# Optimization experiments

Hardware: AMD Instinct MI355X
Metric: run time of the kernel (lower is better)

Reference implementation:

```python
import jax, jax.numpy as jnp
import numpy as np
from jax import lax

B, CR, CS = 2, 256, 512
HR = WR = 64
HS = WS = 32
D_INNER, D_STATE, DT_RANK, D_CONV = 512, 16, 16, 3
EPS = 1e-5


def setup_inputs() -> dict:
    key = jax.random.key(0)
    ks = jax.random.split(key, 16)
    s = 0.02
    return {
        "resnet_feat": jax.random.normal(ks[0], (B, CR, HR, WR), jnp.float32),
        "scp_feat": jax.random.normal(ks[1], (B, CS, HS, WS), jnp.float32),
        "scp_proj_w": jax.random.normal(ks[2], (CR, CS), jnp.float32) * s,
        "scp_bn_g": jnp.ones((CR,), jnp.float32),
        "scp_bn_b": jnp.zeros((CR,), jnp.float32),
        "scp_bn_m": jax.random.normal(ks[3], (CR,), jnp.float32) * 0.1,
        "scp_bn_v": jax.random.uniform(ks[4], (CR,), jnp.float32, minval=0.5, maxval=1.5),
        "res_bn_g": jnp.ones((CR,), jnp.float32),
        "res_bn_b": jnp.zeros((CR,), jnp.float32),
        "res_bn_m": jax.random.normal(ks[5], (CR,), jnp.float32) * 0.1,
        "res_bn_v": jax.random.uniform(ks[6], (CR,), jnp.float32, minval=0.5, maxval=1.5),
        "ln_g": jnp.ones((CR,), jnp.float32),
        "ln_b": jnp.zeros((CR,), jnp.float32),
        "in_proj_w": jax.random.normal(ks[7], (2 * D_INNER, CR), jnp.float32) * s,
        "conv_w": jax.random.normal(ks[8], (D_INNER, 1, D_CONV), jnp.float32) * s,
        "conv_b": jnp.zeros((D_INNER,), jnp.float32),
        "x_proj_w": jax.random.normal(ks[9], (DT_RANK + 2 * D_STATE, D_INNER), jnp.float32) * s,
        "dt_proj_w": jax.random.normal(ks[10], (D_INNER, DT_RANK), jnp.float32) * s,
        "dt_proj_b": jnp.full((D_INNER,), -4.6, jnp.float32),  # softplus -> dt ~ 0.01
        "A_log": jnp.log(jnp.broadcast_to(jnp.arange(1, D_STATE + 1, dtype=jnp.float32), (D_INNER, D_STATE))),
        "D": jnp.ones((D_INNER,), jnp.float32),
        "out_proj_w": jax.random.normal(ks[11], (CR, D_INNER), jnp.float32) * s,
    }


def _bn(x, g, b, m, v):
    # eval-mode BatchNorm2d with running stats, NCHW
    inv = g / jnp.sqrt(v + EPS)
    return x * inv[None, :, None, None] + (b - m * inv)[None, :, None, None]


def reference(resnet_feat, scp_feat, scp_proj_w, scp_bn_g, scp_bn_b, scp_bn_m, scp_bn_v,
              res_bn_g, res_bn_b, res_bn_m, res_bn_v, ln_g, ln_b, in_proj_w, conv_w, conv_b,
              x_proj_w, dt_proj_w, dt_proj_b, A_log, D, out_proj_w):
    # --- fusion prelude ---
    rn = _bn(resnet_feat, res_bn_g, res_bn_b, res_bn_m, res_bn_v)
    sp = jnp.einsum('bchw,oc->bohw', scp_feat, scp_proj_w)        # 1x1 conv, no bias
    sp = _bn(sp, scp_bn_g, scp_bn_b, scp_bn_m, scp_bn_v)
    sp = jax.image.resize(sp, (B, CR, HR, WR), method='bilinear')  # align_corners=False semantics
    fused = rn + sp                                               # (B, CR, HR, WR)

    # --- Mamba2DBlock ---
    L = HR * WR
    x_seq = fused.transpose(0, 2, 3, 1).reshape(B, L, CR)
    mu = x_seq.mean(-1, keepdims=True)
    var = x_seq.var(-1, keepdims=True)
    xn = (x_seq - mu) / jnp.sqrt(var + EPS) * ln_g + ln_b         # LayerNorm

    xz = xn @ in_proj_w.T                                         # (B, L, 2*d_inner)
    xm, z = jnp.split(xz, 2, axis=-1)

    # causal depthwise conv1d over sequence
    xc = xm.transpose(0, 2, 1)                                    # (B, d_inner, L)
    xc = jnp.pad(xc, ((0, 0), (0, 0), (D_CONV - 1, 0)))
    xc = lax.conv_general_dilated(xc, conv_w, (1,), 'VALID',
                                  dimension_numbers=('NCH', 'OIH', 'NCH'),
                                  feature_group_count=D_INNER) + conv_b[None, :, None]
    u = jax.nn.silu(xc.transpose(0, 2, 1))                        # (B, L, d_inner)

    x_dbl = u @ x_proj_w.T                                        # (B, L, dt_rank + 2*d_state)
    dt_in, Bc, Cc = jnp.split(x_dbl, [DT_RANK, DT_RANK + D_STATE], axis=-1)
    dt = jax.nn.softplus(dt_in @ dt_proj_w.T + dt_proj_b)         # (B, L, d_inner)

    A = -jnp.exp(A_log)                                           # (d_inner, d_state)
    dA = jnp.exp(dt[..., None] * A)                               # (B, L, d_inner, d_state)
    dBu = dt[..., None] * Bc[:, :, None, :] * u[..., None]        # (B, L, d_inner, d_state)

    def comb(c1, c2):
        a1, b1 = c1
        a2, b2 = c2
        return a1 * a2, a2 * b1 + b2

    _, h = lax.associative_scan(comb, (dA, dBu), axis=1)          # h: (B, L, d_inner, d_state)
    y = jnp.einsum('blds,bls->bld', h, Cc) + u * D
    y = y * jax.nn.silu(z)
    out_seq = y @ out_proj_w.T                                    # (B, L, CR)
    out = out_seq.reshape(B, HR, WR, CR).transpose(0, 3, 1, 2)
    return fused + out
```

## Files before the change

### kernel.cpp

```cpp
#include <hip/hip_runtime.h>
#include <hip/hip_bf16.h>
#include <math.h>

typedef unsigned short u16;
typedef __attribute__((ext_vector_type(8))) short short8;
typedef __attribute__((ext_vector_type(4))) float f32x4;
typedef __attribute__((ext_vector_type(4))) unsigned short u16x4;

#define DEVINL static __device__ __forceinline__

DEVINL float b2f(u16 x) {
    union { unsigned u; float f; } v; v.u = ((unsigned)x) << 16; return v.f;
}
DEVINL u16 f2b(float f) {
    union { unsigned u; float f; } v; v.f = f;
    unsigned u = v.u;
    return (u16)((u + 0x7fffu + ((u >> 16) & 1u)) >> 16);
}
DEVINL float silu(float x) { return x * __fdividef(1.f, 1.f + __expf(-x)); }
DEVINL float ld_any(bool f32, const void* p, size_t i) {
    return f32 ? ((const float*)p)[i] : b2f(((const u16*)p)[i]);
}
template<bool F32> DEVINL float LDs(const void* p, size_t i) {
    if constexpr (F32) return ((const float*)p)[i];
    else               return b2f(((const u16*)p)[i]);
}

DEVINL bool detect_f32(const u16* __restrict__ raw) {
    int cnt = 0;
#pragma unroll
    for (int i = 0; i < 64; ++i) {
        float v = b2f(raw[i * 2]);
        if (!(fabsf(v) <= 1e3f)) cnt++;
    }
    return cnt > 0;
}

#define O_INW  0
#define O_XPW  262144
#define O_OPW  286720
#define O_SPW  417792
#define O_CW   548864
#define O_CB   550400
#define O_DTW  550912
#define O_ALOG 559104
#define O_DTB  567296
#define O_DW   567808
#define O_SG   568320
#define O_SB   568576
#define O_SM   568832
#define O_SV   569088
#define O_RG   569344
#define O_RB   569600
#define O_RM   569856
#define O_RV   570112
#define O_LG   570368
#define O_LB   570624
#define N_CVT  570880
#define O_FLAG 570880

DEVINL void tr_tile(bool f32, const void* src, u16* dst, int R, int C,
                    int c0, int r0, int b, int tid)
{
    __shared__ u16 t[64][66];
    int lane = tid & 63, grp = tid >> 6;
#pragma unroll
    for (int j = 0; j < 16; ++j) {
        int rl = j * 4 + grp;
        t[rl][lane] = f2b(ld_any(f32, src, ((size_t)b * R + r0 + rl) * C + c0 + lane));
    }
    __syncthreads();
#pragma unroll
    for (int j = 0; j < 16; ++j) {
        int cl = j * 4 + grp;
        dst[((size_t)b * C + c0 + cl) * R + r0 + lane] = t[lane][cl];
    }
}

__global__ __launch_bounds__(256) void k_prep(
    const void* inw, const void* xpw, const void* opw, const void* spw,
    const void* cw, const void* cb, const void* dtw, const void* alog,
    const void* dtb, const void* Dw,
    const void* sg, const void* sb, const void* sm, const void* sv,
    const void* rg, const void* rb, const void* rm, const void* rv,
    const void* lg, const void* lb,
    const void* scp, const void* resnet,
    u16* __restrict__ w16, u16* __restrict__ scpT, u16* __restrict__ resnetT)
{
    bool f32 = detect_f32((const u16*)resnet);
    int bid = blockIdx.x, tid = threadIdx.x;
    if (bid < 2230) {
        int i = bid * 256 + tid;
        const void* src; int off = i;
        if      (i < O_XPW)  { src = inw; }
        else if (i < O_OPW)  { src = xpw;  off = i - O_XPW; }
        else if (i < O_SPW)  { src = opw;  off = i - O_OPW; }
        else if (i < O_CW)   { src = spw;  off = i - O_SPW; }
        else if (i < O_CB)   { src = cw;   off = i - O_CW; }
        else if (i < O_DTW)  { src = cb;   off = i - O_CB; }
        else if (i < O_ALOG) { src = dtw;  off = i - O_DTW; }
        else if (i < O_DTB)  { src = alog; off = i - O_ALOG; }
        else if (i < O_DW)   { src = dtb;  off = i - O_DTB; }
        else if (i < O_SG)   { src = Dw;   off = i - O_DW; }
        else if (i < O_SB)   { src = sg;   off = i - O_SG; }
        else if (i < O_SM)   { src = sb;   off = i - O_SB; }
        else if (i < O_SV)   { src = sm;   off = i - O_SM; }
        else if (i < O_RG)   { src = sv;   off = i - O_SV; }
        else if (i < O_RB)   { src = rg;   off = i - O_RG; }
        else if (i < O_RM)   { src = rb;   off = i - O_RB; }
        else if (i < O_RV)   { src = rm;   off = i - O_RM; }
        else if (i < O_LG)   { src = rv;   off = i - O_RV; }
        else if (i < O_LB)   { src = lg;   off = i - O_LG; }
        else                 { src = lb;   off = i - O_LB; }
        w16[i] = f2b(ld_any(f32, src, off));
    } else if (bid < 2230 + 256) {
        int t = bid - 2230;
        tr_tile(f32, scp, scpT, 512, 1024, (t & 15) * 64, ((t >> 4) & 7) * 64, t >> 7, tid);
    } else if (bid < 2998) {
        int t = bid - 2486;
        tr_tile(f32, resnet, resnetT, 256, 4096, (t & 63) * 64, ((t >> 6) & 3) * 64, t >> 8, tid);
    } else {
        __shared__ int oksh;
        if (tid == 0) oksh = 1;
        __syncthreads();
        bool ok = true;
        for (int i = tid; i < 512 * 16; i += 256) {
            int s = i & 15;
            float av = -__expf(ld_any(f32, alog, i));
            if (fabsf(av + (float)(s + 1)) > 0.03f * (float)(s + 1)) ok = false;
        }
        if (!ok) atomicAnd(&oksh, 0);
        __syncthreads();
        if (tid == 0) w16[O_FLAG] = (u16)oksh;
    }
}

__global__ __launch_bounds__(256) void k_scpmm(
    const u16* __restrict__ scpT, const u16* __restrict__ w16,
    u16* __restrict__ sp16)
{
    const int N = 256, K = 512;
    int tid = threadIdx.x, lane = tid & 63, wid = tid >> 6;
    int ln = lane & 15, q = lane >> 4;
    int m0 = blockIdx.x * 64 + (wid & 1) * 32;
    int n0 = blockIdx.y * 64 + (wid >> 1) * 32;
    f32x4 acc00 = {0.f,0.f,0.f,0.f}, acc01 = acc00, acc10 = acc00, acc11 = acc00;
    const u16* Ap0 = scpT + (size_t)(m0 + ln) * K + q * 8;
    const u16* Ap1 = Ap0 + (size_t)16 * K;
    const u16* Wp = w16 + O_SPW;
#pragma unroll 4
    for (int k0 = 0; k0 < K; k0 += 32) {
        int kk = k0 + q * 8;
        short8 a0 = *reinterpret_cast<const short8*>(Ap0 + k0);
        short8 a1 = *reinterpret_cast<const short8*>(Ap1 + k0);
        short8 b0 = *reinterpret_cast<const short8*>(Wp + (size_t)(n0 + ln) * K + kk);
        short8 b1 = *reinterpret_cast<const short8*>(Wp + (size_t)(n0 + ln + 16) * K + kk);
        acc00 = __builtin_amdgcn_mfma_f32_16x16x32_bf16(a0, b0, acc00, 0, 0, 0);
        acc01 = __builtin_amdgcn_mfma_f32_16x16x32_bf16(a0, b1, acc01, 0, 0, 0);
        acc10 = __builtin_amdgcn_mfma_f32_16x16x32_bf16(a1, b0, acc10, 0, 0, 0);
        acc11 = __builtin_amdgcn_mfma_f32_16x16x32_bf16(a1, b1, acc11, 0, 0, 0);
    }
    int r0 = m0 + q * 4, c0 = n0 + ln;
    float inv0 = b2f(w16[O_SG + c0]) * rsqrtf(b2f(w16[O_SV + c0]) + 1e-5f);
    float sh0  = b2f(w16[O_SB + c0]) - b2f(w16[O_SM + c0]) * inv0;
    float inv1 = b2f(w16[O_SG + c0 + 16]) * rsqrtf(b2f(w16[O_SV + c0 + 16]) + 1e-5f);
    float sh1  = b2f(w16[O_SB + c0 + 16]) - b2f(w16[O_SM + c0 + 16]) * inv1;
#pragma unroll
    for (int r = 0; r < 4; ++r) {
        sp16[(size_t)(r0 + r) * N + c0]           = f2b(acc00[r] * inv0 + sh0);
        sp16[(size_t)(r0 + r) * N + c0 + 16]      = f2b(acc01[r] * inv1 + sh1);
        sp16[(size_t)(r0 + 16 + r) * N + c0]      = f2b(acc10[r] * inv0 + sh0);
        sp16[(size_t)(r0 + 16 + r) * N + c0 + 16] = f2b(acc11[r] * inv1 + sh1);
    }
}

__global__ __launch_bounds__(256) void k_ln(
    const u16* __restrict__ resnetT, const u16* __restrict__ w16,
    const u16* __restrict__ sp16, u16* __restrict__ xn)
{
    __shared__ float red[8];
    int c = threadIdx.x, b = blockIdx.y;
    float inv = b2f(w16[O_RG + c]) * rsqrtf(b2f(w16[O_RV + c]) + 1e-5f);
    float sh  = b2f(w16[O_RB + c]) - b2f(w16[O_RM + c]) * inv;
    float lgv = b2f(w16[O_LG + c]), lbv = b2f(w16[O_LB + c]);
    const u16* spc = sp16 + (size_t)b * 1024 * 256 + c;
    for (int j = 0; j < 8; ++j) {
        int l = blockIdx.x * 8 + j;
        int h = l >> 6, w = l & 63;
        float rr = b2f(resnetT[((size_t)b * 4096 + l) * 256 + c]);
        float rn = rr * inv + sh;
        float xh = 0.5f * h - 0.25f; int jh = (int)floorf(xh); float fh = xh - jh;
        float xw = 0.5f * w - 0.25f; int jw = (int)floorf(xw); float fw = xw - jw;
        int h0 = jh < 0 ? 0 : jh, h1 = jh + 1 > 31 ? 31 : jh + 1;
        int w0 = jw < 0 ? 0 : jw, w1 = jw + 1 > 31 ? 31 : jw + 1;
        float v00 = b2f(spc[(size_t)(h0 * 32 + w0) * 256]), v01 = b2f(spc[(size_t)(h0 * 32 + w1) * 256]);
        float v10 = b2f(spc[(size_t)(h1 * 32 + w0) * 256]), v11 = b2f(spc[(size_t)(h1 * 32 + w1) * 256]);
        float sp = (1.f - fh) * ((1.f - fw) * v00 + fw * v01)
                 + fh * ((1.f - fw) * v10 + fw * v11);
        float fv = rn + sp;

        float s = fv, s2 = fv * fv;
#pragma unroll
        for (int off = 1; off < 64; off <<= 1) {
            s  += __shfl_xor(s, off);
            s2 += __shfl_xor(s2, off);
        }
        int wv = c >> 6;
        if ((c & 63) == 0) { red[wv] = s; red[4 + wv] = s2; }
        __syncthreads();
        float S  = red[0] + red[1] + red[2] + red[3];
        float S2 = red[4] + red[5] + red[6] + red[7];
        __syncthreads();
        float mu   = S * (1.f / 256.f);
        float var  = S2 * (1.f / 256.f) - mu * mu;
        float rstd = rsqrtf(var + 1e-5f);
        xn[((size_t)b * 4096 + l) * 256 + c] = f2b((fv - mu) * rstd * lgv + lbv);
    }
}

__global__ __launch_bounds__(256) void k_gemm_in(
    const u16* __restrict__ A, const u16* __restrict__ w16, u16* __restrict__ Out)
{
    const int N = 1024, K = 256;
    int tid = threadIdx.x, lane = tid & 63, wid = tid >> 6;
    int ln = lane & 15, q = lane >> 4;
    int m0 = blockIdx.x * 128 + (wid & 1) * 64;
    int n0 = blockIdx.y * 128 + (wid >> 1) * 64;
    f32x4 acc[4][4];
#pragma unroll
    for (int i = 0; i < 4; ++i)
#pragma unroll
        for (int j = 0; j < 4; ++j) acc[i][j] = {0.f,0.f,0.f,0.f};
    const u16* Ap = A + (size_t)(m0 + ln) * K + q * 8;
    const u16* Bp = w16 + O_INW + (size_t)(n0 + ln) * K + q * 8;
#pragma unroll
    for (int k0 = 0; k0 < K; k0 += 32) {
        short8 a[4], bb[4];
#pragma unroll
        for (int i = 0; i < 4; ++i)
            a[i] = *reinterpret_cast<const short8*>(Ap + (size_t)(16 * i) * K + k0);
#pragma unroll
        for (int j = 0; j < 4; ++j)
            bb[j] = *reinterpret_cast<const short8*>(Bp + (size_t)(16 * j) * K + k0);
#pragma unroll
        for (int i = 0; i < 4; ++i)
#pragma unroll
            for (int j = 0; j < 4; ++j)
                acc[i][j] = __builtin_amdgcn_mfma_f32_16x16x32_bf16(a[i], bb[j], acc[i][j], 0, 0, 0);
    }
    int r0 = m0 + q * 4, c0 = n0 + ln;
#pragma unroll
    for (int i = 0; i < 4; ++i)
#pragma unroll
        for (int j = 0; j < 4; ++j)
#pragma unroll
            for (int r = 0; r < 4; ++r)
                Out[(size_t)(r0 + 16 * i + r) * N + c0 + 16 * j] = f2b(acc[i][j][r]);
}

DEVINL short8 u_frag(const u16* __restrict__ xz, const u16* __restrict__ w16,
                     int row, int kk0)
{
    int l = row & 4095;
    const u16* p = xz + (size_t)row * 1024 + kk0;
    short8 zz = {0,0,0,0,0,0,0,0};
    short8 x0 = *reinterpret_cast<const short8*>(p);
    short8 x1 = (l >= 1) ? *reinterpret_cast<const short8*>(p - 1024) : zz;
    short8 x2 = (l >= 2) ? *reinterpret_cast<const short8*>(p - 2048) : zz;
    short8 r;
#pragma unroll
    for (int j = 0; j < 8; ++j) {
        int d = kk0 + j;
        float acc = b2f(w16[O_CB + d])
                  + b2f((u16)x2[j]) * b2f(w16[O_CW + d * 3])
                  + b2f((u16)x1[j]) * b2f(w16[O_CW + d * 3 + 1])
                  + b2f((u16)x0[j]) * b2f(w16[O_CW + d * 3 + 2]);
        r[j] = (short)f2b(silu(acc));
    }
    return r;
}

__global__ __launch_bounds__(128) void k_xproj(
    const u16* __restrict__ xz, const u16* __restrict__ w16, float* __restrict__ xdf)
{
    int tid = threadIdx.x, lane = tid & 63, wid = tid >> 6;
    int ln = lane & 15, q = lane >> 4;
    int m0 = blockIdx.x * 32 + wid * 16;
    const u16* Wp = w16 + O_XPW;
    f32x4 acc[3];
#pragma unroll
    for (int j = 0; j < 3; ++j) acc[j] = {0.f,0.f,0.f,0.f};
    for (int k0 = 0; k0 < 512; k0 += 32) {
        int kk0 = k0 + q * 8;
        short8 a0 = u_frag(xz, w16, m0 + ln, kk0);
#pragma unroll
        for (int j = 0; j < 3; ++j) {
            short8 bj = *reinterpret_cast<const short8*>(Wp + (size_t)(16 * j + ln) * 512 + kk0);
            acc[j] = __builtin_amdgcn_mfma_f32_16x16x32_bf16(a0, bj, acc[j], 0, 0, 0);
        }
    }
#pragma unroll
    for (int j = 0; j < 3; ++j)
#pragma unroll
        for (int r = 0; r < 4; ++r)
            xdf[(size_t)(m0 + q * 4 + r) * 48 + 16 * j + ln] = acc[j][r];
}


#define SCAN_PRELUDE()                                                        \
    const float* xr = xr0 + (size_t)il * 48;                                  \
    float x0 = b2f(xz[xbase + (size_t)il * 1024]);                            \
    float uv = silu(cbv + cw0 * x2 + cw1 * x1 + cw2 * x0);                    \
    float pa = 0.f, pb = 0.f, pc = 0.f, pq = 0.f;                             \
    _Pragma("unroll")                                                         \
    for (int j = 0; j < 4; ++j) {                                             \
        pa += xr[j]      * wdt[j];      pb += xr[4 + j]  * wdt[4 + j];        \
        pc += xr[8 + j]  * wdt[8 + j];  pq += xr[12 + j] * wdt[12 + j];       \
    }                                                                         \
    float accd = bias + ((pa + pb) + (pc + pq));                              \
    float dtv = accd > 15.f ? accd : __logf(1.f + __expf(accd));              \
    float du = dtv * uv;

__global__ __launch_bounds__(512) void k_scan1(
    const u16* __restrict__ xz, const float* __restrict__ xdf,
    const u16* __restrict__ w16, unsigned* __restrict__ cAH,
    int NC, int CL)
{
    int d = threadIdx.x, ck = blockIdx.x, b = blockIdx.y;
    float wdt[16];
#pragma unroll
    for (int j = 0; j < 16; ++j) wdt[j] = b2f(w16[O_DTW + d * 16 + j]);
    float bias = b2f(w16[O_DTB + d]);
    float cw0 = b2f(w16[O_CW + d * 3]), cw1 = b2f(w16[O_CW + d * 3 + 1]),
          cw2 = b2f(w16[O_CW + d * 3 + 2]), cbv = b2f(w16[O_CB + d]);
    int l0 = ck * CL;
    size_t xbase = ((size_t)b * 4096 + l0) * 1024 + d;
    float x2 = (l0 >= 2) ? b2f(xz[xbase - 2048]) : 0.f;
    float x1 = (l0 >= 1) ? b2f(xz[xbase - 1024]) : 0.f;
    const float* xr0 = xdf + ((size_t)b * 4096 + l0) * 48;
    size_t obase = (((size_t)b * NC + ck) * 16) * 512 + d;
    float h[16];
#pragma unroll
    for (int s = 0; s < 16; ++s) h[s] = 0.f;

    if (w16[O_FLAG]) {
        float sdt = 0.f;
#pragma unroll 2
        for (int il = 0; il < CL; ++il) {
            SCAN_PRELUDE();
            sdt += dtv;
            float e1 = __expf(-dtv);
            float e2 = e1 * e1, e3 = e2 * e1, e4 = e2 * e2;
            float e8 = e4 * e4, e12 = e8 * e4;
            float inn[4] = {e1, e2, e3, e4};
            float bas[4] = {1.f, e4, e8, e12};
#pragma unroll
            for (int s = 0; s < 16; ++s)
                h[s] = (bas[s >> 2] * inn[s & 3]) * h[s] + du * xr[16 + s];
            x2 = x1; x1 = x0;
        }
        float E1 = __expf(-sdt);
        float E2 = E1 * E1, E3 = E2 * E1, E4 = E2 * E2;
        float E8 = E4 * E4, E12 = E8 * E4;
        float iN[4] = {E1, E2, E3, E4};
        float bA[4] = {1.f, E4, E8, E12};
#pragma unroll
        for (int s = 0; s < 16; ++s)
            cAH[obase + (size_t)s * 512] =
                (unsigned)f2b(bA[s >> 2] * iN[s & 3]) | ((unsigned)f2b(h[s]) << 16);
    } else {
        float a[16], ap[16];
#pragma unroll
        for (int s = 0; s < 16; ++s) {
            a[s] = -__expf(b2f(w16[O_ALOG + d * 16 + s]));
            ap[s] = 1.f;
        }
        for (int il = 0; il < CL; ++il) {
            SCAN_PRELUDE();
#pragma unroll
            for (int s = 0; s < 16; ++s) {
                float dA = __expf(dtv * a[s]);
                h[s] = dA * h[s] + du * xr[16 + s];
                ap[s] *= dA;
            }
            x2 = x1; x1 = x0;
        }
#pragma unroll
        for (int s = 0; s < 16; ++s)
            cAH[obase + (size_t)s * 512] =
                (unsigned)f2b(ap[s]) | ((unsigned)f2b(h[s]) << 16);
    }
}

__global__ __launch_bounds__(128) void k_scan2(
    const unsigned* __restrict__ cAH, u16* __restrict__ hIn, int NC)
{
    int d = blockIdx.y * 128 + threadIdx.x, s = blockIdx.x, b = blockIdx.z;
    float h = 0.f;
#pragma unroll 8
    for (int ck = 0; ck < NC; ++ck) {
        size_t idx = (((size_t)b * NC + ck) * 16 + s) * 512 + d;
        unsigned v = cAH[idx];
        float aP = b2f((u16)(v & 0xffffu));
        float hE = b2f((u16)(v >> 16));
        hIn[idx] = f2b(h);
        h = aP * h + hE;
    }
}

__global__ __launch_bounds__(512) void k_scan3(
    const u16* __restrict__ xz, const float* __restrict__ xdf,
    const u16* __restrict__ w16, const u16* __restrict__ hIn,
    u16* __restrict__ y, int NC, int CL)
{
    int d = threadIdx.x, ck = blockIdx.x, b = blockIdx.y;
    float wdt[16];
#pragma unroll
    for (int j = 0; j < 16; ++j) wdt[j] = b2f(w16[O_DTW + d * 16 + j]);
    float bias = b2f(w16[O_DTB + d]);
    float Dv = b2f(w16[O_DW + d]);
    float cw0 = b2f(w16[O_CW + d * 3]), cw1 = b2f(w16[O_CW + d * 3 + 1]),
          cw2 = b2f(w16[O_CW + d * 3 + 2]), cbv = b2f(w16[O_CB + d]);
    int l0 = ck * CL;
    size_t xbase = ((size_t)b * 4096 + l0) * 1024 + d;
    float x2 = (l0 >= 2) ? b2f(xz[xbase - 2048]) : 0.f;
    float x1 = (l0 >= 1) ? b2f(xz[xbase - 1024]) : 0.f;
    const float* xr0 = xdf + ((size_t)b * 4096 + l0) * 48;
    size_t obase = (((size_t)b * NC + ck) * 16) * 512 + d;
    float h[16];
#pragma unroll
    for (int s = 0; s < 16; ++s) h[s] = b2f(hIn[obase + (size_t)s * 512]);

    if (w16[O_FLAG]) {
#pragma unroll 2
        for (int il = 0; il < CL; ++il) {
            SCAN_PRELUDE();
            float e1 = __expf(-dtv);
            float e2 = e1 * e1, e3 = e2 * e1, e4 = e2 * e2;
            float e8 = e4 * e4, e12 = e8 * e4;
            float inn[4] = {e1, e2, e3, e4};
            float bas[4] = {1.f, e4, e8, e12};
            float yv = 0.f;
#pragma unroll
            for (int s = 0; s < 16; ++s) {
                h[s] = (bas[s >> 2] * inn[s & 3]) * h[s] + du * xr[16 + s];
                yv += h[s] * xr[32 + s];
            }
            size_t row = (size_t)b * 4096 + l0 + il;
            yv += uv * Dv;
            float zv = b2f(xz[row * 1024 + 512 + d]);
            yv *= silu(zv);
            y[row * 512 + d] = f2b(yv);
            x2 = x1; x1 = x0;
        }
    } else {
        float a[16];
#pragma unroll
        for (int s = 0; s < 16; ++s)
            a[s] = -__expf(b2f(w16[O_ALOG + d * 16 + s]));
        for (int il = 0; il < CL; ++il) {
            SCAN_PRELUDE();
            float yv = 0.f;
#pragma unroll
            for (int s = 0; s < 16; ++s) {
                float dA = __expf(dtv * a[s]);
                h[s] = dA * h[s] + du * xr[16 + s];
                yv += h[s] * xr[32 + s];
            }
            size_t row = (size_t)b * 4096 + l0 + il;
            yv += uv * Dv;
            float zv = b2f(xz[row * 1024 + 512 + d]);
            yv *= silu(zv);
            y[row * 512 + d] = f2b(yv);
            x2 = x1; x1 = x0;
        }
    }
}

template<bool F32> DEVINL void out_body(
    const u16* Y, const u16* w16, const void* resnet,
    const u16* sp16, void* outp)
{
    const int K = 512;
    int tid = threadIdx.x, lane = tid & 63, wid = tid >> 6;
    int ln = lane & 15, q = lane >> 4;
    int m0 = blockIdx.x * 64 + (wid & 1) * 32;
    int n0 = blockIdx.y * 128 + (wid >> 1) * 64;
    f32x4 acc[2][4];
#pragma unroll
    for (int i = 0; i < 2; ++i)
#pragma unroll
        for (int j = 0; j < 4; ++j) acc[i][j] = {0.f,0.f,0.f,0.f};
    const u16* Ap0 = w16 + O_OPW + (size_t)(m0 + ln) * K + q * 8;
    const u16* Ap1 = Ap0 + (size_t)16 * K;
    const u16* Bp  = Y + (size_t)(n0 + ln) * K + q * 8;
#pragma unroll 2
    for (int k0 = 0; k0 < K; k0 += 32) {
        short8 a0 = *reinterpret_cast<const short8*>(Ap0 + k0);
        short8 a1 = *reinterpret_cast<const short8*>(Ap1 + k0);
#pragma unroll
        for (int j = 0; j < 4; ++j) {
            short8 bj = *reinterpret_cast<const short8*>(Bp + (size_t)(16 * j) * K + k0);
            acc[0][j] = __builtin_amdgcn_mfma_f32_16x16x32_bf16(a0, bj, acc[0][j], 0, 0, 0);
            acc[1][j] = __builtin_amdgcn_mfma_f32_16x16x32_bf16(a1, bj, acc[1][j], 0, 0, 0);
        }
    }
    int r0 = m0 + q * 4;
    int nb = n0 + ln;
    float inv8[2][4], sh8[2][4];
#pragma unroll
    for (int im = 0; im < 2; ++im)
#pragma unroll
        for (int r = 0; r < 4; ++r) {
            int c = r0 + 16 * im + r;
            float inv = b2f(w16[O_RG + c]) * rsqrtf(b2f(w16[O_RV + c]) + 1e-5f);
            inv8[im][r] = inv;
            sh8[im][r]  = b2f(w16[O_RB + c]) - b2f(w16[O_RM + c]) * inv;
        }
#pragma unroll
    for (int jn = 0; jn < 4; ++jn) {
        int n = nb + 16 * jn;
        int b = n >> 12, l = n & 4095;
        int hh = l >> 6, w = l & 63;
        float xh = 0.5f * hh - 0.25f; int jh = (int)floorf(xh); float fh = xh - jh;
        float xw = 0.5f * w - 0.25f;  int jw = (int)floorf(xw); float fw = xw - jw;
        int h0 = jh < 0 ? 0 : jh, h1 = jh + 1 > 31 ? 31 : jh + 1;
        int w0 = jw < 0 ? 0 : jw, w1 = jw + 1 > 31 ? 31 : jw + 1;
        float w00 = (1.f - fh) * (1.f - fw), w01 = (1.f - fh) * fw;
        float w10 = fh * (1.f - fw),         w11 = fh * fw;
        const u16* spb = sp16 + (size_t)b * 1024 * 256;
#pragma unroll
        for (int im = 0; im < 2; ++im) {
            int cb = r0 + 16 * im;
            u16x4 s00 = *reinterpret_cast<const u16x4*>(spb + (size_t)(h0 * 32 + w0) * 256 + cb);
            u16x4 s01 = *reinterpret_cast<const u16x4*>(spb + (size_t)(h0 * 32 + w1) * 256 + cb);
            u16x4 s10 = *reinterpret_cast<const u16x4*>(spb + (size_t)(h1 * 32 + w0) * 256 + cb);
            u16x4 s11 = *reinterpret_cast<const u16x4*>(spb + (size_t)(h1 * 32 + w1) * 256 + cb);
#pragma unroll
            for (int r = 0; r < 4; ++r) {
                int c = cb + r;
                float rr = LDs<F32>(resnet, ((size_t)b * 256 + c) * 4096 + l);
                float sp = w00 * b2f(s00[r]) + w01 * b2f(s01[r])
                         + w10 * b2f(s10[r]) + w11 * b2f(s11[r]);
                float val = acc[im][jn][r] + rr * inv8[im][r] + sh8[im][r] + sp;
                size_t oi = ((size_t)b * 256 + c) * 4096 + l;
                if constexpr (F32) ((float*)outp)[oi] = val;
                else               ((u16*)outp)[oi]  = f2b(val);
            }
        }
    }
}
__global__ __launch_bounds__(256) void k_out(
    const u16* Y, const u16* w16, const void* resnet,
    const u16* sp16, void* outp)
{
    if (detect_f32((const u16*)resnet)) out_body<true>(Y, w16, resnet, sp16, outp);
    else                                out_body<false>(Y, w16, resnet, sp16, outp);
}

extern "C" void kernel_launch(void* const* d_in, const int* in_sizes, int n_in,
                              void* d_out, int out_size, void* d_ws, size_t ws_size,
                              hipStream_t stream)
{
    const void* resnet = d_in[0];
    const void* scp    = d_in[1];
    const void* spw    = d_in[2];
    const void* sg     = d_in[3];
    const void* sb     = d_in[4];
    const void* sm     = d_in[5];
    const void* sv     = d_in[6];
    const void* rg     = d_in[7];
    const void* rb     = d_in[8];
    const void* rm     = d_in[9];
    const void* rv     = d_in[10];
    const void* lg     = d_in[11];
    const void* lb     = d_in[12];
    const void* inw    = d_in[13];
    const void* cw     = d_in[14];
    const void* cb     = d_in[15];
    const void* xpw    = d_in[16];
    const void* dtw    = d_in[17];
    const void* dtb    = d_in[18];
    const void* alog   = d_in[19];
    const void* Dw     = d_in[20];
    const void* opw    = d_in[21];

    char*  ws      = (char*)d_ws;
    u16*   w16     = (u16*)(ws + 4096);
    u16*   sp16    = (u16*)(ws + 2097152);
    u16*   scpT    = (u16*)(ws + 4194304);
    u16*   resnetT = (u16*)(ws + 8388608);
    u16*   xn      = (u16*)(ws + 12582912);
    u16*   xz      = (u16*)(ws + 16777216);
    float* xdf     = (float*)(ws + 33554432);
    u16*   y       = (u16*)(ws + 35651584);
    const size_t tail0 = 44040192;

    int NC = 16;
    for (int cand = 256; cand >= 16; cand >>= 1) {
        if (tail0 + (size_t)cand * 98304 <= ws_size) { NC = cand; break; }
    }
    int CL = 4096 / NC;
    unsigned* cAH = (unsigned*)(ws + tail0);
    u16*      hIn = (u16*)(ws + tail0 + (size_t)NC * 65536);

    k_prep<<<dim3(2999), 256, 0, stream>>>(
        inw, xpw, opw, spw, cw, cb, dtw, alog, dtb, Dw,
        sg, sb, sm, sv, rg, rb, rm, rv, lg, lb,
        scp, resnet, w16, scpT, resnetT);
    k_scpmm<<<dim3(32, 4), 256, 0, stream>>>(scpT, w16, sp16);
    k_ln<<<dim3(512, 2), 256, 0, stream>>>(resnetT, w16, sp16, xn);
    k_gemm_in<<<dim3(64, 8), 256, 0, stream>>>(xn, w16, xz);
    k_xproj<<<dim3(256), 128, 0, stream>>>(xz, w16, xdf);
    k_scan1<<<dim3(NC, 2), 512, 0, stream>>>(xz, xdf, w16, cAH, NC, CL);
    k_scan2<<<dim3(16, 4, 2), 128, 0, stream>>>(cAH, hIn, NC);
    k_scan3<<<dim3(NC, 2), 512, 0, stream>>>(xz, xdf, w16, hIn, y, NC, CL);
    k_out<<<dim3(4, 64), 256, 0, stream>>>(y, w16, resnet, sp16, d_out);
}
```

Before: 250.3 us.

## Fuse all pipeline stages into one cooperative persistent kernel with grid syncs

Replaces nine separate kernel launches with a single cooperative kernel of 512 blocks of 512 threads. Every phase (prep, scp GEMM, LayerNorm, in-proj GEMM, x-proj, three scan passes, output) is remapped onto that fixed grid, with grid.sync between phases. Tile shapes are reworked to fit: gemm_in and out use narrower N tiles, and x-proj splits K across 4 waves with a shared-memory reduction. The scan chunk count is fixed at 256 instead of being chosen from workspace size. The aim is to remove launch gaps and tail effects, at the cost of grid-wide barriers, idle blocks in small phases, and 512-thread/occupancy register limits; there is a non-cooperative multi-launch fallback.

```diff
diff --git a/kernel.cpp b/kernel.cpp
--- a/kernel.cpp
+++ b/kernel.cpp
@@ -1,4 +1,5 @@
 #include <hip/hip_runtime.h>
+#include <hip/hip_cooperative_groups.h>
 #include <hip/hip_bf16.h>
 #include <math.h>
 
@@ -59,93 +60,102 @@
 #define N_CVT  570880
 #define O_FLAG 570880
 
-DEVINL void tr_tile(bool f32, const void* src, u16* dst, int R, int C,
-                    int c0, int r0, int b, int tid)
-{
-    __shared__ u16 t[64][66];
+#define NCK 256
+#define CLL 16
+
+struct KP {
+    const void *resnet, *scp, *spw, *sg, *sb, *sm, *sv, *rg, *rb, *rm, *rv,
+               *lg, *lb, *inw, *cw, *cb, *xpw, *dtw, *dtb, *alog, *Dw, *opw;
+    u16 *w16, *scpT, *resnetT, *xn, *sp16, *xz, *y, *hIn;
+    float *xdf;
+    unsigned *cAH;
+    void *outp;
+};
+
+DEVINL void tr_tile8(bool f32, const void* src, u16* dst, int R, int C,
+                     int c0, int r0, int b, int tid, u16 (*t)[66])
+{
     int lane = tid & 63, grp = tid >> 6;
 #pragma unroll
-    for (int j = 0; j < 16; ++j) {
-        int rl = j * 4 + grp;
+    for (int j = 0; j < 8; ++j) {
+        int rl = j * 8 + grp;
         t[rl][lane] = f2b(ld_any(f32, src, ((size_t)b * R + r0 + rl) * C + c0 + lane));
     }
     __syncthreads();
 #pragma unroll
-    for (int j = 0; j < 16; ++j) {
-        int cl = j * 4 + grp;
+    for (int j = 0; j < 8; ++j) {
+        int cl = j * 8 + grp;
         dst[((size_t)b * C + c0 + cl) * R + r0 + lane] = t[lane][cl];
     }
 }
 
-__global__ __launch_bounds__(256) void k_prep(
-    const void* inw, const void* xpw, const void* opw, const void* spw,
-    const void* cw, const void* cb, const void* dtw, const void* alog,
-    const void* dtb, const void* Dw,
-    const void* sg, const void* sb, const void* sm, const void* sv,
-    const void* rg, const void* rb, const void* rm, const void* rv,
-    const void* lg, const void* lb,
-    const void* scp, const void* resnet,
-    u16* __restrict__ w16, u16* __restrict__ scpT, u16* __restrict__ resnetT)
-{
-    bool f32 = detect_f32((const u16*)resnet);
-    int bid = blockIdx.x, tid = threadIdx.x;
-    if (bid < 2230) {
-        int i = bid * 256 + tid;
-        const void* src; int off = i;
-        if      (i < O_XPW)  { src = inw; }
-        else if (i < O_OPW)  { src = xpw;  off = i - O_XPW; }
-        else if (i < O_SPW)  { src = opw;  off = i - O_OPW; }
-        else if (i < O_CW)   { src = spw;  off = i - O_SPW; }
-        else if (i < O_CB)   { src = cw;   off = i - O_CW; }
-        else if (i < O_DTW)  { src = cb;   off = i - O_CB; }
-        else if (i < O_ALOG) { src = dtw;  off = i - O_DTW; }
-        else if (i < O_DTB)  { src = alog; off = i - O_ALOG; }
-        else if (i < O_DW)   { src = dtb;  off = i - O_DTB; }
-        else if (i < O_SG)   { src = Dw;   off = i - O_DW; }
-        else if (i < O_SB)   { src = sg;   off = i - O_SG; }
-        else if (i < O_SM)   { src = sb;   off = i - O_SB; }
-        else if (i < O_SV)   { src = sm;   off = i - O_SM; }
-        else if (i < O_RG)   { src = sv;   off = i - O_SV; }
-        else if (i < O_RB)   { src = rg;   off = i - O_RG; }
-        else if (i < O_RM)   { src = rb;   off = i - O_RB; }
-        else if (i < O_RV)   { src = rm;   off = i - O_RM; }
-        else if (i < O_LG)   { src = rv;   off = i - O_RV; }
-        else if (i < O_LB)   { src = lg;   off = i - O_LG; }
-        else                 { src = lb;   off = i - O_LB; }
-        w16[i] = f2b(ld_any(f32, src, off));
-    } else if (bid < 2230 + 256) {
-        int t = bid - 2230;
-        tr_tile(f32, scp, scpT, 512, 1024, (t & 15) * 64, ((t >> 4) & 7) * 64, t >> 7, tid);
-    } else if (bid < 2998) {
-        int t = bid - 2486;
-        tr_tile(f32, resnet, resnetT, 256, 4096, (t & 63) * 64, ((t >> 6) & 3) * 64, t >> 8, tid);
-    } else {
-        __shared__ int oksh;
-        if (tid == 0) oksh = 1;
+DEVINL void ph_prep(const KP& P, int blk, int tid, bool f32,
+                    u16 (*t)[66], int* sh_ok)
+{
+    u16* __restrict__ w16 = P.w16;
+    for (int id = blk; id < 1884; id += 512) {
+        if (id < 1115) {
+            int i = id * 512 + tid;
+            const void* src; int off = i;
+            if      (i < O_XPW)  { src = P.inw; }
+            else if (i < O_OPW)  { src = P.xpw;  off = i - O_XPW; }
+            else if (i < O_SPW)  { src = P.opw;  off = i - O_OPW; }
+            else if (i < O_CW)   { src = P.spw;  off = i - O_SPW; }
+            else if (i < O_CB)   { src = P.cw;   off = i - O_CW; }
+            else if (i < O_DTW)  { src = P.cb;   off = i - O_CB; }
+            else if (i < O_ALOG) { src = P.dtw;  off = i - O_DTW; }
+            else if (i < O_DTB)  { src = P.alog; off = i - O_ALOG; }
+            else if (i < O_DW)   { src = P.dtb;  off = i - O_DTB; }
+            else if (i < O_SG)   { src = P.Dw;   off = i - O_DW; }
+            else if (i < O_SB)   { src = P.sg;   off = i - O_SG; }
+            else if (i < O_SM)   { src = P.sb;   off = i - O_SB; }
+            else if (i < O_SV)   { src = P.sm;   off = i - O_SM; }
+            else if (i < O_RG)   { src = P.sv;   off = i - O_SV; }
+            else if (i < O_RB)   { src = P.rg;   off = i - O_RG; }
+            else if (i < O_RM)   { src = P.rb;   off = i - O_RB; }
+            else if (i < O_RV)   { src = P.rm;   off = i - O_RM; }
+            else if (i < O_LG)   { src = P.rv;   off = i - O_RV; }
+            else if (i < O_LB)   { src = P.lg;   off = i - O_LG; }
+            else                 { src = P.lb;   off = i - O_LB; }
+            w16[i] = f2b(ld_any(f32, src, off));
+        } else if (id < 1371) {
+            int tt = id - 1115;
+            tr_tile8(f32, P.scp, P.scpT, 512, 1024,
+                     (tt & 15) * 64, ((tt >> 4) & 7) * 64, tt >> 7, tid, t);
+        } else if (id < 1883) {
+            int tt = id - 1371;
+            tr_tile8(f32, P.resnet, P.resnetT, 256, 4096,
+                     (tt & 63) * 64, ((tt >> 6) & 3) * 64, tt >> 8, tid, t);
+        } else {
+            if (tid == 0) *sh_ok = 1;
+            __syncthreads();
+            bool ok = true;
+            for (int i = tid; i < 512 * 16; i += 512) {
+                int s = i & 15;
+                float av = -__expf(ld_any(f32, P.alog, i));
+                if (fabsf(av + (float)(s + 1)) > 0.03f * (float)(s + 1)) ok = false;
+            }
+            if (!ok) atomicAnd(sh_ok, 0);
+            __syncthreads();
+            if (tid == 0) w16[O_FLAG] = (u16)(*sh_ok);
+        }
         __syncthreads();
-        bool ok = true;
-        for (int i = tid; i < 512 * 16; i += 256) {
-            int s = i & 15;
-            float av = -__expf(ld_any(f32, alog, i));
-            if (fabsf(av + (float)(s + 1)) > 0.03f * (float)(s + 1)) ok = false;
-        }
-        if (!ok) atomicAnd(&oksh, 0);
-        __syncthreads();
-        if (tid == 0) w16[O_FLAG] = (u16)oksh;
-    }
-}
-
-__global__ __launch_bounds__(256) void k_scpmm(
-    const u16* __restrict__ scpT, const u16* __restrict__ w16,
-    u16* __restrict__ sp16)
-{
+    }
+}
+
+DEVINL void ph_scpmm(const KP& P, int blk, int tid)
+{
+    if (blk >= 128) return;
+    int lane = tid & 63, wid = tid >> 6;
+    if (wid >= 4) return;
+    const u16* __restrict__ w16 = P.w16;
     const int N = 256, K = 512;
-    int tid = threadIdx.x, lane = tid & 63, wid = tid >> 6;
     int ln = lane & 15, q = lane >> 4;
-    int m0 = blockIdx.x * 64 + (wid & 1) * 32;
-    int n0 = blockIdx.y * 64 + (wid >> 1) * 32;
+    int bx = blk & 31, by = blk >> 5;
+    int m0 = bx * 64 + (wid & 1) * 32;
+    int n0 = by * 64 + (wid >> 1) * 32;
     f32x4 acc00 = {0.f,0.f,0.f,0.f}, acc01 = acc00, acc10 = acc00, acc11 = acc00;
-    const u16* Ap0 = scpT + (size_t)(m0 + ln) * K + q * 8;
+    const u16* Ap0 = P.scpT + (size_t)(m0 + ln) * K + q * 8;
     const u16* Ap1 = Ap0 + (size_t)16 * K;
     const u16* Wp = w16 + O_SPW;
 #pragma unroll 4
@@ -167,27 +177,25 @@
     float sh1  = b2f(w16[O_SB + c0 + 16]) - b2f(w16[O_SM + c0 + 16]) * inv1;
 #pragma unroll
     for (int r = 0; r < 4; ++r) {
-        sp16[(size_t)(r0 + r) * N + c0]           = f2b(acc00[r] * inv0 + sh0);
-        sp16[(size_t)(r0 + r) * N + c0 + 16]      = f2b(acc01[r] * inv1 + sh1);
-        sp16[(size_t)(r0 + 16 + r) * N + c0]      = f2b(acc10[r] * inv0 + sh0);
-        sp16[(size_t)(r0 + 16 + r) * N + c0 + 16] = f2b(acc11[r] * inv1 + sh1);
-    }
-}
-
-__global__ __launch_bounds__(256) void k_ln(
-    const u16* __restrict__ resnetT, const u16* __restrict__ w16,
-    const u16* __restrict__ sp16, u16* __restrict__ xn)
-{
-    __shared__ float red[8];
-    int c = threadIdx.x, b = blockIdx.y;
+        P.sp16[(size_t)(r0 + r) * N + c0]           = f2b(acc00[r] * inv0 + sh0);
+        P.sp16[(size_t)(r0 + r) * N + c0 + 16]      = f2b(acc01[r] * inv1 + sh1);
+        P.sp16[(size_t)(r0 + 16 + r) * N + c0]      = f2b(acc10[r] * inv0 + sh0);
+        P.sp16[(size_t)(r0 + 16 + r) * N + c0 + 16] = f2b(acc11[r] * inv1 + sh1);
+    }
+}
+
+DEVINL void ph_ln(const KP& P, int blk, int tid, float (*red)[8])
+{
+    const u16* __restrict__ w16 = P.w16;
+    int sub = tid >> 8, c = tid & 255, b = sub;
     float inv = b2f(w16[O_RG + c]) * rsqrtf(b2f(w16[O_RV + c]) + 1e-5f);
     float sh  = b2f(w16[O_RB + c]) - b2f(w16[O_RM + c]) * inv;
     float lgv = b2f(w16[O_LG + c]), lbv = b2f(w16[O_LB + c]);
-    const u16* spc = sp16 + (size_t)b * 1024 * 256 + c;
+    const u16* spc = P.sp16 + (size_t)b * 1024 * 256 + c;
     for (int j = 0; j < 8; ++j) {
-        int l = blockIdx.x * 8 + j;
+        int l = blk * 8 + j;
         int h = l >> 6, w = l & 63;
-        float rr = b2f(resnetT[((size_t)b * 4096 + l) * 256 + c]);
+        float rr = b2f(P.resnetT[((size_t)b * 4096 + l) * 256 + c]);
         float rn = rr * inv + sh;
         float xh = 0.5f * h - 0.25f; int jh = (int)floorf(xh); float fh = xh - jh;
         float xw = 0.5f * w - 0.25f; int jw = (int)floorf(xw); float fw = xw - jw;
@@ -206,56 +214,56 @@
             s2 += __shfl_xor(s2, off);
         }
         int wv = c >> 6;
-        if ((c & 63) == 0) { red[wv] = s; red[4 + wv] = s2; }
+        if ((c & 63) == 0) { red[sub][wv] = s; red[sub][4 + wv] = s2; }
         __syncthreads();
-        float S  = red[0] + red[1] + red[2] + red[3];
-        float S2 = red[4] + red[5] + red[6] + red[7];
+        float S  = red[sub][0] + red[sub][1] + red[sub][2] + red[sub][3];
+        float S2 = red[sub][4] + red[sub][5] + red[sub][6] + red[sub][7];
         __syncthreads();
         float mu   = S * (1.f / 256.f);
         float var  = S2 * (1.f / 256.f) - mu * mu;
         float rstd = rsqrtf(var + 1e-5f);
-        xn[((size_t)b * 4096 + l) * 256 + c] = f2b((fv - mu) * rstd * lgv + lbv);
-    }
-}
-
-__global__ __launch_bounds__(256) void k_gemm_in(
-    const u16* __restrict__ A, const u16* __restrict__ w16, u16* __restrict__ Out)
-{
-    const int N = 1024, K = 256;
-    int tid = threadIdx.x, lane = tid & 63, wid = tid >> 6;
+        P.xn[((size_t)b * 4096 + l) * 256 + c] = f2b((fv - mu) * rstd * lgv + lbv);
+    }
+}
+
+DEVINL void ph_gemm_in(const KP& P, int blk, int tid)
+{
+    const int Nn = 1024, K = 256;
+    int lane = tid & 63, wid = tid >> 6;
     int ln = lane & 15, q = lane >> 4;
-    int m0 = blockIdx.x * 128 + (wid & 1) * 64;
-    int n0 = blockIdx.y * 128 + (wid >> 1) * 64;
-    f32x4 acc[4][4];
+    int bx = blk & 63, by = blk >> 6;
+    int m0 = bx * 128 + (wid & 1) * 64;
+    int n0 = by * 128 + (wid >> 1) * 32;
+    f32x4 acc[4][2];
 #pragma unroll
     for (int i = 0; i < 4; ++i)
 #pragma unroll
-        for (int j = 0; j < 4; ++j) acc[i][j] = {0.f,0.f,0.f,0.f};
-    const u16* Ap = A + (size_t)(m0 + ln) * K + q * 8;
-    const u16* Bp = w16 + O_INW + (size_t)(n0 + ln) * K + q * 8;
+        for (int j = 0; j < 2; ++j) acc[i][j] = {0.f,0.f,0.f,0.f};
+    const u16* Ap = P.xn + (size_t)(m0 + ln) * K + q * 8;
+    const u16* Bp = P.w16 + O_INW + (size_t)(n0 + ln) * K + q * 8;
 #pragma unroll
     for (int k0 = 0; k0 < K; k0 += 32) {
-        short8 a[4], bb[4];
+        short8 a[4], bb[2];
 #pragma unroll
         for (int i = 0; i < 4; ++i)
             a[i] = *reinterpret_cast<const short8*>(Ap + (size_t)(16 * i) * K + k0);
 #pragma unroll
-        for (int j = 0; j < 4; ++j)
+        for (int j = 0; j < 2; ++j)
             bb[j] = *reinterpret_cast<const short8*>(Bp + (size_t)(16 * j) * K + k0);
 #pragma unroll
         for (int i = 0; i < 4; ++i)
 #pragma unroll
-            for (int j = 0; j < 4; ++j)
+            for (int j = 0; j < 2; ++j)
                 acc[i][j] = __builtin_amdgcn_mfma_f32_16x16x32_bf16(a[i], bb[j], acc[i][j], 0, 0, 0);
     }
     int r0 = m0 + q * 4, c0 = n0 + ln;
 #pragma unroll
     for (int i = 0; i < 4; ++i)
 #pragma unroll
-        for (int j = 0; j < 4; ++j)
+        for (int j = 0; j < 2; ++j)
 #pragma unroll
             for (int r = 0; r < 4; ++r)
-                Out[(size_t)(r0 + 16 * i + r) * N + c0 + 16 * j] = f2b(acc[i][j][r]);
+                P.xz[(size_t)(r0 + 16 * i + r) * Nn + c0 + 16 * j] = f2b(acc[i][j][r]);
 }
 
 DEVINL short8 u_frag(const u16* __restrict__ xz, const u16* __restrict__ w16,
@@ -280,19 +288,21 @@
     return r;
 }
 
-__global__ __launch_bounds__(128) void k_xproj(
-    const u16* __restrict__ xz, const u16* __restrict__ w16, float* __restrict__ xdf)
-{
-    int tid = threadIdx.x, lane = tid & 63, wid = tid >> 6;
+DEVINL void ph_xproj(const KP& P, int blk, int tid, float (*xred)[4][64][12])
+{
+    if (blk >= 256) return;
+    int lane = tid & 63, wid = tid >> 6;
     int ln = lane & 15, q = lane >> 4;
-    int m0 = blockIdx.x * 32 + wid * 16;
-    const u16* Wp = w16 + O_XPW;
+    int grp = wid >> 2, wsub = wid & 3;
+    int m0 = blk * 32 + grp * 16;
+    const u16* Wp = P.w16 + O_XPW;
     f32x4 acc[3];
 #pragma unroll
     for (int j = 0; j < 3; ++j) acc[j] = {0.f,0.f,0.f,0.f};
-    for (int k0 = 0; k0 < 512; k0 += 32) {
+    int kb = wsub * 128;
+    for (int k0 = kb; k0 < kb + 128; k0 += 32) {
         int kk0 = k0 + q * 8;
-        short8 a0 = u_frag(xz, w16, m0 + ln, kk0);
+        short8 a0 = u_frag(P.xz, P.w16, m0 + ln, kk0);
 #pragma unroll
         for (int j = 0; j < 3; ++j) {
             short8 bj = *reinterpret_cast<const short8*>(Wp + (size_t)(16 * j + ln) * 512 + kk0);
@@ -302,10 +312,19 @@
 #pragma unroll
     for (int j = 0; j < 3; ++j)
 #pragma unroll
-        for (int r = 0; r < 4; ++r)
-            xdf[(size_t)(m0 + q * 4 + r) * 48 + 16 * j + ln] = acc[j][r];
-}
-
+        for (int r = 0; r < 4; ++r) xred[grp][wsub][lane][j * 4 + r] = acc[j][r];
+    __syncthreads();
+    if (wsub == 0) {
+#pragma unroll
+        for (int j = 0; j < 3; ++j)
+#pragma unroll
+            for (int r = 0; r < 4; ++r) {
+                float v = xred[grp][0][lane][j * 4 + r] + xred[grp][1][lane][j * 4 + r]
+                        + xred[grp][2][lane][j * 4 + r] + xred[grp][3][lane][j * 4 + r];
+                P.xdf[(size_t)(m0 + q * 4 + r) * 48 + 16 * j + ln] = v;
+            }
+    }
+}
 
 #define SCAN_PRELUDE()                                                        \
     const float* xr = xr0 + (size_t)il * 48;                                  \
@@ -321,24 +340,23 @@
     float dtv = accd > 15.f ? accd : __logf(1.f + __expf(accd));              \
     float du = dtv * uv;
 
-__global__ __launch_bounds__(512) void k_scan1(
-    const u16* __restrict__ xz, const float* __restrict__ xdf,
-    const u16* __restrict__ w16, unsigned* __restrict__ cAH,
-    int NC, int CL)
-{
-    int d = threadIdx.x, ck = blockIdx.x, b = blockIdx.y;
+DEVINL void ph_scan1(const KP& P, int blk, int tid)
+{
+    const u16* __restrict__ w16 = P.w16;
+    const u16* __restrict__ xz = P.xz;
+    int d = tid, ck = blk & 255, b = blk >> 8;
     float wdt[16];
 #pragma unroll
     for (int j = 0; j < 16; ++j) wdt[j] = b2f(w16[O_DTW + d * 16 + j]);
     float bias = b2f(w16[O_DTB + d]);
     float cw0 = b2f(w16[O_CW + d * 3]), cw1 = b2f(w16[O_CW + d * 3 + 1]),
           cw2 = b2f(w16[O_CW + d * 3 + 2]), cbv = b2f(w16[O_CB + d]);
-    int l0 = ck * CL;
+    int l0 = ck * CLL;
     size_t xbase = ((size_t)b * 4096 + l0) * 1024 + d;
     float x2 = (l0 >= 2) ? b2f(xz[xbase - 2048]) : 0.f;
     float x1 = (l0 >= 1) ? b2f(xz[xbase - 1024]) : 0.f;
-    const float* xr0 = xdf + ((size_t)b * 4096 + l0) * 48;
-    size_t obase = (((size_t)b * NC + ck) * 16) * 512 + d;
+    const float* xr0 = P.xdf + ((size_t)b * 4096 + l0) * 48;
+    size_t obase = (((size_t)b * NCK + ck) * 16) * 512 + d;
     float h[16];
 #pragma unroll
     for (int s = 0; s < 16; ++s) h[s] = 0.f;
@@ -346,7 +364,7 @@
     if (w16[O_FLAG]) {
         float sdt = 0.f;
 #pragma unroll 2
-        for (int il = 0; il < CL; ++il) {
+        for (int il = 0; il < CLL; ++il) {
             SCAN_PRELUDE();
             sdt += dtv;
             float e1 = __expf(-dtv);
@@ -366,7 +384,7 @@
         float bA[4] = {1.f, E4, E8, E12};
 #pragma unroll
         for (int s = 0; s < 16; ++s)
-            cAH[obase + (size_t)s * 512] =
+            P.cAH[obase + (size_t)s * 512] =
                 (unsigned)f2b(bA[s >> 2] * iN[s & 3]) | ((unsigned)f2b(h[s]) << 16);
     } else {
         float a[16], ap[16];
@@ -375,7 +393,7 @@
             a[s] = -__expf(b2f(w16[O_ALOG + d * 16 + s]));
             ap[s] = 1.f;
         }
-        for (int il = 0; il < CL; ++il) {
+        for (int il = 0; il < CLL; ++il) {
             SCAN_PRELUDE();
 #pragma unroll
             for (int s = 0; s < 16; ++s) {
@@ -387,33 +405,32 @@
         }
 #pragma unroll
         for (int s = 0; s < 16; ++s)
-            cAH[obase + (size_t)s * 512] =
+            P.cAH[obase + (size_t)s * 512] =
                 (unsigned)f2b(ap[s]) | ((unsigned)f2b(h[s]) << 16);
     }
 }
 
-__global__ __launch_bounds__(128) void k_scan2(
-    const unsigned* __restrict__ cAH, u16* __restrict__ hIn, int NC)
-{
-    int d = blockIdx.y * 128 + threadIdx.x, s = blockIdx.x, b = blockIdx.z;
+DEVINL void ph_scan2(const KP& P, int blk, int tid)
+{
+    if (blk >= 32) return;
+    int b = blk >> 4, s = blk & 15, d = tid;
     float h = 0.f;
 #pragma unroll 8
-    for (int ck = 0; ck < NC; ++ck) {
-        size_t idx = (((size_t)b * NC + ck) * 16 + s) * 512 + d;
-        unsigned v = cAH[idx];
+    for (int ck = 0; ck < NCK; ++ck) {
+        size_t idx = (((size_t)b * NCK + ck) * 16 + s) * 512 + d;
+        unsigned v = P.cAH[idx];
         float aP = b2f((u16)(v & 0xffffu));
         float hE = b2f((u16)(v >> 16));
-        hIn[idx] = f2b(h);
+        P.hIn[idx] = f2b(h);
         h = aP * h + hE;
     }
 }
 
-__global__ __launch_bounds__(512) void k_scan3(
-    const u16* __restrict__ xz, const float* __restrict__ xdf,
-    const u16* __restrict__ w16, const u16* __restrict__ hIn,
-    u16* __restrict__ y, int NC, int CL)
-{
-    int d = threadIdx.x, ck = blockIdx.x, b = blockIdx.y;
+DEVINL void ph_scan3(const KP& P, int blk, int tid)
+{
+    const u16* __restrict__ w16 = P.w16;
+    const u16* __restrict__ xz = P.xz;
+    int d = tid, ck = blk & 255, b = blk >> 8;
     float wdt[16];
 #pragma unroll
     for (int j = 0; j < 16; ++j) wdt[j] = b2f(w16[O_DTW + d * 16 + j]);
@@ -421,19 +438,19 @@
     float Dv = b2f(w16[O_DW + d]);
     float cw0 = b2f(w16[O_CW + d * 3]), cw1 = b2f(w16[O_CW + d * 3 + 1]),
           cw2 = b2f(w16[O_CW + d * 3 + 2]), cbv = b2f(w16[O_CB + d]);
-    int l0 = ck * CL;
+    int l0 = ck * CLL;
     size_t xbase = ((size_t)b * 4096 + l0) * 1024 + d;
     float x2 = (l0 >= 2) ? b2f(xz[xbase - 2048]) : 0.f;
     float x1 = (l0 >= 1) ? b2f(xz[xbase - 1024]) : 0.f;
-    const float* xr0 = xdf + ((size_t)b * 4096 + l0) * 48;
-    size_t obase = (((size_t)b * NC + ck) * 16) * 512 + d;
+    const float* xr0 = P.xdf + ((size_t)b * 4096 + l0) * 48;
+    size_t obase = (((size_t)b * NCK + ck) * 16) * 512 + d;
     float h[16];
 #pragma unroll
-    for (int s = 0; s < 16; ++s) h[s] = b2f(hIn[obase + (size_t)s * 512]);
+    for (int s = 0; s < 16; ++s) h[s] = b2f(P.hIn[obase + (size_t)s * 512]);
 
     if (w16[O_FLAG]) {
 #pragma unroll 2
-        for (int il = 0; il < CL; ++il) {
+        for (int il = 0; il < CLL; ++il) {
             SCAN_PRELUDE();
             float e1 = __expf(-dtv);
             float e2 = e1 * e1, e3 = e2 * e1, e4 = e2 * e2;
@@ -450,7 +467,7 @@
             yv += uv * Dv;
             float zv = b2f(xz[row * 1024 + 512 + d]);
             yv *= silu(zv);
-            y[row * 512 + d] = f2b(yv);
+            P.y[row * 512 + d] = f2b(yv);
             x2 = x1; x1 = x0;
         }
     } else {
@@ -458,7 +475,7 @@
 #pragma unroll
         for (int s = 0; s < 16; ++s)
             a[s] = -__expf(b2f(w16[O_ALOG + d * 16 + s]));
-        for (int il = 0; il < CL; ++il) {
+        for (int il = 0; il < CLL; ++il) {
             SCAN_PRELUDE();
             float yv = 0.f;
 #pragma unroll
@@ -471,39 +488,41 @@
             yv += uv * Dv;
             float zv = b2f(xz[row * 1024 + 512 + d]);
             yv *= silu(zv);
-            y[row * 512 + d] = f2b(yv);
+            P.y[row * 512 + d] = f2b(yv);
             x2 = x1; x1 = x0;
         }
     }
 }
 
-template<bool F32> DEVINL void out_body(
-    const u16* Y, const u16* w16, const void* resnet,
-    const u16* sp16, void* outp)
-{
+template<bool F32> DEVINL void ph_out(const KP& P, int blk, int tid)
+{
+    if (blk >= 256) return;
+    const u16* __restrict__ w16 = P.w16;
     const int K = 512;
-    int tid = threadIdx.x, lane = tid & 63, wid = tid >> 6;
+    int lane = tid & 63, wid = tid >> 6;
     int ln = lane & 15, q = lane >> 4;
-    int m0 = blockIdx.x * 64 + (wid & 1) * 32;
-    int n0 = blockIdx.y * 128 + (wid >> 1) * 64;
-    f32x4 acc[2][4];
+    int fx = blk & 3, fy = blk >> 2;
+    int m0 = fx * 64 + (wid & 1) * 32;
+    int n0 = fy * 128 + (wid >> 1) * 32;
+    f32x4 acc[2][2];
 #pragma unroll
     for (int i = 0; i < 2; ++i)
 #pragma unroll
-        for (int j = 0; j < 4; ++j) acc[i][j] = {0.f,0.f,0.f,0.f};
+        for (int j = 0; j < 2; ++j) acc[i][j] = {0.f,0.f,0.f,0.f};
     const u16* Ap0 = w16 + O_OPW + (size_t)(m0 + ln) * K + q * 8;
     const u16* Ap1 = Ap0 + (size_t)16 * K;
-    const u16* Bp  = Y + (size_t)(n0 + ln) * K + q * 8;
+    const u16* Bp0 = P.y + (size_t)(n0 + ln) * K + q * 8;
+    const u16* Bp1 = Bp0 + (size_t)16 * K;
 #pragma unroll 2
     for (int k0 = 0; k0 < K; k0 += 32) {
         short8 a0 = *reinterpret_cast<const short8*>(Ap0 + k0);
         short8 a1 = *reinterpret_cast<const short8*>(Ap1 + k0);
-#pragma unroll
-        for (int j = 0; j < 4; ++j) {
-            short8 bj = *reinterpret_cast<const short8*>(Bp + (size_t)(16 * j) * K + k0);
-            acc[0][j] = __builtin_amdgcn_mfma_f32_16x16x32_bf16(a0, bj, acc[0][j], 0, 0, 0);
-            acc[1][j] = __builtin_amdgcn_mfma_f32_16x16x32_bf16(a1, bj, acc[1][j], 0, 0, 0);
-        }
+        short8 b0 = *reinterpret_cast<const short8*>(Bp0 + k0);
+        short8 b1 = *reinterpret_cast<const short8*>(Bp1 + k0);
+        acc[0][0] = __builtin_amdgcn_mfma_f32_16x16x32_bf16(a0, b0, acc[0][0], 0, 0, 0);
+        acc[0][1] = __builtin_amdgcn_mfma_f32_16x16x32_bf16(a0, b1, acc[0][1], 0, 0, 0);
+        acc[1][0] = __builtin_amdgcn_mfma_f32_16x16x32_bf16(a1, b0, acc[1][0], 0, 0, 0);
+        acc[1][1] = __builtin_amdgcn_mfma_f32_16x16x32_bf16(a1, b1, acc[1][1], 0, 0, 0);
     }
     int r0 = m0 + q * 4;
     int nb = n0 + ln;
@@ -518,7 +537,7 @@
             sh8[im][r]  = b2f(w16[O_RB + c]) - b2f(w16[O_RM + c]) * inv;
         }
 #pragma unroll
-    for (int jn = 0; jn < 4; ++jn) {
+    for (int jn = 0; jn < 2; ++jn) {
         int n = nb + 16 * jn;
         int b = n >> 12, l = n & 4095;
         int hh = l >> 6, w = l & 63;
@@ -528,7 +547,7 @@
         int w0 = jw < 0 ? 0 : jw, w1 = jw + 1 > 31 ? 31 : jw + 1;
         float w00 = (1.f - fh) * (1.f - fw), w01 = (1.f - fh) * fw;
         float w10 = fh * (1.f - fw),         w11 = fh * fw;
-        const u16* spb = sp16 + (size_t)b * 1024 * 256;
+        const u16* spb = P.sp16 + (size_t)b * 1024 * 256;
 #pragma unroll
         for (int im = 0; im < 2; ++im) {
             int cb = r0 + 16 * im;
@@ -539,81 +558,127 @@
 #pragma unroll
             for (int r = 0; r < 4; ++r) {
                 int c = cb + r;
-                float rr = LDs<F32>(resnet, ((size_t)b * 256 + c) * 4096 + l);
+                float rr = LDs<F32>(P.resnet, ((size_t)b * 256 + c) * 4096 + l);
                 float sp = w00 * b2f(s00[r]) + w01 * b2f(s01[r])
                          + w10 * b2f(s10[r]) + w11 * b2f(s11[r]);
                 float val = acc[im][jn][r] + rr * inv8[im][r] + sh8[im][r] + sp;
                 size_t oi = ((size_t)b * 256 + c) * 4096 + l;
-                if constexpr (F32) ((float*)outp)[oi] = val;
-                else               ((u16*)outp)[oi]  = f2b(val);
+                if constexpr (F32) ((float*)P.outp)[oi] = val;
+                else               ((u16*)P.outp)[oi]  = f2b(val);
             }
         }
     }
 }
-__global__ __launch_bounds__(256) void k_out(
-    const u16* Y, const u16* w16, const void* resnet,
-    const u16* sp16, void* outp)
-{
-    if (detect_f32((const u16*)resnet)) out_body<true>(Y, w16, resnet, sp16, outp);
-    else                                out_body<false>(Y, w16, resnet, sp16, outp);
+
+__global__ __launch_bounds__(512, 4) void k_mega(KP P)
+{
+    namespace cg = cooperative_groups;
+    cg::grid_group grid = cg::this_grid();
+    __shared__ u16 sh_t[64][66];
+    __shared__ float sh_red[2][8];
+    __shared__ float sh_xred[2][4][64][12];
+    __shared__ int sh_ok;
+
+    const int blk = blockIdx.x, tid = threadIdx.x;
+    const bool f32 = detect_f32((const u16*)P.resnet);
+
+    ph_prep(P, blk, tid, f32, sh_t, &sh_ok);
+    grid.sync();
+    ph_scpmm(P, blk, tid);
+    grid.sync();
+    ph_ln(P, blk, tid, sh_red);
+    grid.sync();
+    ph_gemm_in(P, blk, tid);
+    grid.sync();
+    ph_xproj(P, blk, tid, sh_xred);
+    grid.sync();
+    ph_scan1(P, blk, tid);
+    grid.sync();
+    ph_scan2(P, blk, tid);
+    grid.sync();
+    ph_scan3(P, blk, tid);
+    grid.sync();
+    if (f32) ph_out<true>(P, blk, tid);
+    else     ph_out<false>(P, blk, tid);
+}
+
+__global__ __launch_bounds__(512, 4) void k_p0(KP P) {
+    __shared__ u16 sh_t[64][66]; __shared__ int sh_ok;
+    ph_prep(P, blockIdx.x, threadIdx.x, detect_f32((const u16*)P.resnet), sh_t, &sh_ok);
+}
+__global__ __launch_bounds__(512, 4) void k_p1(KP P) { ph_scpmm(P, blockIdx.x, threadIdx.x); }
+__global__ __launch_bounds__(512, 4) void k_p2(KP P) {
+    __shared__ float sh_red[2][8];
+    ph_ln(P, blockIdx.x, threadIdx.x, sh_red);
+}
+__global__ __launch_bounds__(512, 4) void k_p3(KP P) { ph_gemm_in(P, blockIdx.x, threadIdx.x); }
+__global__ __launch_bounds__(512, 4) void k_p4(KP P) {
+    __shared__ float sh_xred[2][4][64][12];
+    ph_xproj(P, blockIdx.x, threadIdx.x, sh_xred);
+}
+__global__ __launch_bounds__(512, 4) void k_p5(KP P) { ph_scan1(P, blockIdx.x, threadIdx.x); }
+__global__ __launch_bounds__(512, 4) void k_p6(KP P) { ph_scan2(P, blockIdx.x, threadIdx.x); }
+__global__ __launch_bounds__(512, 4) void k_p7(KP P) { ph_scan3(P, blockIdx.x, threadIdx.x); }
+__global__ __launch_bounds__(512, 4) void k_p8(KP P) {
+    if (detect_f32((const u16*)P.resnet)) ph_out<true>(P, blockIdx.x, threadIdx.x);
+    else                                  ph_out<false>(P, blockIdx.x, threadIdx.x);
 }
 
 extern "C" void kernel_launch(void* const* d_in, const int* in_sizes, int n_in,
                               void* d_out, int out_size, void* d_ws, size_t ws_size,
                               hipStream_t stream)
 {
-    const void* resnet = d_in[0];
-    const void* scp    = d_in[1];
-    const void* spw    = d_in[2];
-    const void* sg     = d_in[3];
-    const void* sb     = d_in[4];
-    const void* sm     = d_in[5];
-    const void* sv     = d_in[6];
-    const void* rg     = d_in[7];
-    const void* rb     = d_in[8];
-    const void* rm     = d_in[9];
-    const void* rv     = d_in[10];
-    const void* lg     = d_in[11];
-    const void* lb     = d_in[12];
-    const void* inw    = d_in[13];
-    const void* cw     = d_in[14];
-    const void* cb     = d_in[15];
-    const void* xpw    = d_in[16];
-    const void* dtw    = d_in[17];
-    const void* dtb    = d_in[18];
-    const void* alog   = d_in[19];
-    const void* Dw     = d_in[20];
-    const void* opw    = d_in[21];
-
-    char*  ws      = (char*)d_ws;
-    u16*   w16     = (u16*)(ws + 4096);
-    u16*   sp16    = (u16*)(ws + 2097152);
-    u16*   scpT    = (u16*)(ws + 4194304);
-    u16*   resnetT = (u16*)(ws + 8388608);
-    u16*   xn      = (u16*)(ws + 12582912);
-    u16*   xz      = (u16*)(ws + 16777216);
-    float* xdf     = (float*)(ws + 33554432);
-    u16*   y       = (u16*)(ws + 35651584);
+    KP P;
+    P.resnet = d_in[0];
+    P.scp    = d_in[1];
+    P.spw    = d_in[2];
+    P.sg     = d_in[3];
+    P.sb     = d_in[4];
+    P.sm     = d_in[5];
+    P.sv     = d_in[6];
+    P.rg     = d_in[7];
+    P.rb     = d_in[8];
+    P.rm     = d_in[9];
+    P.rv     = d_in[10];
+    P.lg     = d_in[11];
+    P.lb     = d_in[12];
+    P.inw    = d_in[13];
+    P.cw     = d_in[14];
+    P.cb     = d_in[15];
+    P.xpw    = d_in[16];
+    P.dtw    = d_in[17];
+    P.dtb    = d_in[18];
+    P.alog   = d_in[19];
+    P.Dw     = d_in[20];
+    P.opw    = d_in[21];
+
+    char* ws  = (char*)d_ws;
+    P.w16     = (u16*)(ws + 4096);
+    P.sp16    = (u16*)(ws + 2097152);
+    P.scpT    = (u16*)(ws + 4194304);
+    P.resnetT = (u16*)(ws + 8388608);
+    P.xn      = (u16*)(ws + 12582912);
+    P.xz      = (u16*)(ws + 16777216);
+    P.xdf     = (float*)(ws + 33554432);
+    P.y       = (u16*)(ws + 35651584);
     const size_t tail0 = 44040192;
-
-    int NC = 16;
-    for (int cand = 256; cand >= 16; cand >>= 1) {
-        if (tail0 + (size_t)cand * 98304 <= ws_size) { NC = cand; break; }
-    }
-    int CL = 4096 / NC;
-    unsigned* cAH = (unsigned*)(ws + tail0);
-    u16*      hIn = (u16*)(ws + tail0 + (size_t)NC * 65536);
-
-    k_prep<<<dim3(2999), 256, 0, stream>>>(
-        inw, xpw, opw, spw, cw, cb, dtw, alog, dtb, Dw,
-        sg, sb, sm, sv, rg, rb, rm, rv, lg, lb,
-        scp, resnet, w16, scpT, resnetT);
-    k_scpmm<<<dim3(32, 4), 256, 0, stream>>>(scpT, w16, sp16);
-    k_ln<<<dim3(512, 2), 256, 0, stream>>>(resnetT, w16, sp16, xn);
-    k_gemm_in<<<dim3(64, 8), 256, 0, stream>>>(xn, w16, xz);
-    k_xproj<<<dim3(256), 128, 0, stream>>>(xz, w16, xdf);
-    k_scan1<<<dim3(NC, 2), 512, 0, stream>>>(xz, xdf, w16, cAH, NC, CL);
-    k_scan2<<<dim3(16, 4, 2), 128, 0, stream>>>(cAH, hIn, NC);
-    k_scan3<<<dim3(NC, 2), 512, 0, stream>>>(xz, xdf, w16, hIn, y, NC, CL);
-    k_out<<<dim3(4, 64), 256, 0, stream>>>(y, w16, resnet, sp16, d_out);
-}
+    P.cAH     = (unsigned*)(ws + tail0);
+    P.hIn     = (u16*)(ws + tail0 + (size_t)NCK * 65536);
+    P.outp    = d_out;
+
+    void* args[] = { (void*)&P };
+    hipError_t err = hipLaunchCooperativeKernel(
+        (const void*)k_mega, dim3(512), dim3(512), args, 0, stream);
+    if (err != hipSuccess) {
+        (void)hipGetLastError();
+        k_p0<<<dim3(512), dim3(512), 0, stream>>>(P);
+        k_p1<<<dim3(512), dim3(512), 0, stream>>>(P);
+        k_p2<<<dim3(512), dim3(512), 0, stream>>>(P);
+        k_p3<<<dim3(512), dim3(512), 0, stream>>>(P);
+        k_p4<<<dim3(512), dim3(512), 0, stream>>>(P);
+        k_p5<<<dim3(512), dim3(512), 0, stream>>>(P);
+        k_p6<<<dim3(512), dim3(512), 0, stream>>>(P);
+        k_p7<<<dim3(512), dim3(512), 0, stream>>>(P);
+        k_p8<<<dim3(512), dim3(512), 0, stream>>>(P);
+    }
+}
```

New measurement: 751.1 us. 200% more time.
